# Kernel optimization log

Measured on AMD Instinct MI355X. Metric: run time of the kernel, lower is better.

The kernel has to match this reference:

```python
import jax, jax.numpy as jnp
import numpy as np

NEG_INF = -9e15
NEG_SLOPE = 0.2

def setup_inputs() -> dict:
    key = jax.random.key(0)
    k1, k2, k3, k4 = jax.random.split(key, 4)
    N, d_in, d_out = 8192, 256, 256
    x = jax.random.normal(k1, (N, d_in), dtype=jnp.float32)
    adj = jax.random.randint(k2, (N, N), 0, 2).astype(jnp.float32)
    W = jax.random.normal(k3, (d_in, d_out), dtype=jnp.float32) * (1.0 / np.sqrt(d_in))
    a = jax.random.normal(k4, (2 * d_out,), dtype=jnp.float32) * (1.0 / np.sqrt(2 * d_out))
    return {"x": x, "adj": adj, "W": W, "a": a}

def reference(x, adj, W, a):
    d_out = W.shape[1]
    Wh = x @ W                                   # [N, d_out]
    # a([Wh_i || Wh_j]) decomposed: e_ij = <a_src, Wh_i> + <a_dst, Wh_j>
    e_src = Wh @ a[:d_out]                       # [N]
    e_dst = Wh @ a[d_out:]                       # [N]
    e = jax.nn.leaky_relu(e_src[:, None] + e_dst[None, :], NEG_SLOPE)  # [N, N]
    N = Wh.shape[0]
    mask = (adj > 0) | jnp.eye(N, dtype=bool)
    e = jnp.where(mask, e, NEG_INF)
    alpha = jax.nn.softmax(e, axis=1)            # [N, N]
    h = alpha @ Wh                               # [N, d_out]
    return h
```

## Files before the change

kernel.cpp:

```cpp
#include <hip/hip_runtime.h>
#include <stdint.h>

#define N 8192
#define D 256

typedef __attribute__((ext_vector_type(4))) float f32x4;
typedef __attribute__((ext_vector_type(8))) short bf16x8;

__device__ __forceinline__ unsigned short f2bf(float f) {
    unsigned u = __float_as_uint(f);
    u += 0x7fff + ((u >> 16) & 1);
    return (unsigned short)(u >> 16);
}
__device__ __forceinline__ float leaky(float x) {
    return fmaxf(x, 0.f) + 0.2f * fminf(x, 0.f);
}
__device__ __forceinline__ void sync_lds() {
    asm volatile("s_waitcnt lgkmcnt(0)\n\ts_barrier" ::: "memory");
}

__global__ __launch_bounds__(256) void k0_compress(const float* __restrict__ adj,
                                                   unsigned int* __restrict__ mask) {
    const size_t fbase = ((size_t)blockIdx.x * 256 + threadIdx.x) * 4;
    float4 v = *(const float4*)(adj + fbase);
    const int lane = threadIdx.x & 63;
    unsigned nib = (v.x > 0.f ? 1u : 0u) | (v.y > 0.f ? 2u : 0u) |
                   (v.z > 0.f ? 4u : 0u) | (v.w > 0.f ? 8u : 0u);
    unsigned word = nib << ((lane & 7) * 4);
    word |= __shfl_xor(word, 1);
    word |= __shfl_xor(word, 2);
    word |= __shfl_xor(word, 4);
    if ((lane & 7) == 0) {
        size_t widx = fbase >> 5;
        int r = (int)(widx >> 8);
        int ww = (int)(widx & 255);
        if ((r >> 5) == ww) word |= 1u << (r & 31);
        mask[widx] = word;
    }
}

#define K1_BM 8
__global__ __launch_bounds__(256) void k1_gemm(const float* __restrict__ x,
                                               const float* __restrict__ W,
                                               float* __restrict__ Wh,
                                               unsigned short* __restrict__ WhT) {
    __shared__ float xsT[32][12];
    const int t = threadIdx.x;
    const int r0 = blockIdx.x * K1_BM;
    float acc[K1_BM];
#pragma unroll
    for (int i = 0; i < K1_BM; ++i) acc[i] = 0.f;

    for (int k0 = 0; k0 < D; k0 += 32) {
        __syncthreads();
        if (t < 64) {
            int r = t >> 3, ks = (t & 7) * 4;
            float4 v = *(const float4*)(x + (size_t)(r0 + r) * D + k0 + ks);
            xsT[ks + 0][r] = v.x; xsT[ks + 1][r] = v.y;
            xsT[ks + 2][r] = v.z; xsT[ks + 3][r] = v.w;
        }
        __syncthreads();
#pragma unroll 8
        for (int kk = 0; kk < 32; ++kk) {
            float wv = W[(size_t)(k0 + kk) * D + t];
#pragma unroll
            for (int rc = 0; rc < K1_BM / 4; ++rc) {
                float4 xv = *(const float4*)&xsT[kk][rc * 4];
                acc[rc * 4 + 0] += xv.x * wv;
                acc[rc * 4 + 1] += xv.y * wv;
                acc[rc * 4 + 2] += xv.z * wv;
                acc[rc * 4 + 3] += xv.w * wv;
            }
        }
    }
#pragma unroll
    for (int r = 0; r < K1_BM; ++r) Wh[(size_t)(r0 + r) * D + t] = acc[r];
    unsigned short pk[K1_BM];
#pragma unroll
    for (int r = 0; r < K1_BM; ++r) pk[r] = f2bf(acc[r]);
    uint4* dst = (uint4*)(WhT + (size_t)t * N + r0);
    dst[0] = *(uint4*)&pk[0];
}

__global__ __launch_bounds__(256) void k2_edot(const float* __restrict__ Wh,
                                               const float* __restrict__ a,
                                               float* __restrict__ e_src,
                                               float* __restrict__ e_dst) {
    const int wave = threadIdx.x >> 6, lane = threadIdx.x & 63;
    const int row = blockIdx.x * 4 + wave;
    float4 wv = *(const float4*)(Wh + (size_t)row * D + lane * 4);
    float4 as = *(const float4*)(a + lane * 4);
    float4 ad = *(const float4*)(a + D + lane * 4);
    float ps = wv.x * as.x + wv.y * as.y + wv.z * as.z + wv.w * as.w;
    float pd = wv.x * ad.x + wv.y * ad.y + wv.z * ad.z + wv.w * ad.w;
#pragma unroll
    for (int m = 1; m < 64; m <<= 1) {
        ps += __shfl_xor(ps, m);
        pd += __shfl_xor(pd, m);
    }
    if (lane == 0) { e_src[row] = ps; e_dst[row] = pd; }
}

__global__ __launch_bounds__(256) void k3_max(const float* __restrict__ e_dst,
                                              float* __restrict__ maxdst) {
    __shared__ float red[4];
    const int t = threadIdx.x;
    float m = -3.4e38f;
    for (int i = t; i < N; i += 256) m = fmaxf(m, e_dst[i]);
#pragma unroll
    for (int msk = 1; msk < 64; msk <<= 1) m = fmaxf(m, __shfl_xor(m, msk));
    if ((t & 63) == 0) red[t >> 6] = m;
    __syncthreads();
    if (t == 0) *maxdst = fmaxf(fmaxf(red[0], red[1]), fmaxf(red[2], red[3]));
}

#define BM 64
#define BK 64
#define RB (N / BM)
#define SPLITS 8
#define NITER ((N / SPLITS) / BK)
#define PSTRIDE 72
__global__ __launch_bounds__(512, 4) void k4_main(const unsigned char* __restrict__ mask,
                                                  const unsigned short* __restrict__ WhT,
                                                  const float* __restrict__ e_src,
                                                  const float* __restrict__ e_dst,
                                                  const float* __restrict__ maxdst,
                                                  float* __restrict__ O_part,
                                                  float* __restrict__ l_part) {
    __shared__ unsigned short p_lds[2][BM][PSTRIDE];

    const int t = threadIdx.x;
    const int rb = blockIdx.x & (RB - 1);
    const int s  = blockIdx.x >> 7;
    const int r0 = rb * BM;
    const int j0 = s * (N / SPLITS);

    const int pr = t >> 3;
    const int pcw = t & 7;
    const int pc = pcw * 8;
    const int gr = r0 + pr;

    const int w = t >> 6;
    const int lane = t & 63;
    const int quad = lane >> 4, lo = lane & 15;

    const float md = *maxdst;
    const float es = e_src[gr];
    const float m = leaky(es + md);

    f32x4 acc[4][2];
#pragma unroll
    for (int mt = 0; mt < 4; ++mt)
#pragma unroll
        for (int nt = 0; nt < 2; ++nt)
            acc[mt][nt] = (f32x4){0.f, 0.f, 0.f, 0.f};
    float lsum = 0.f;

    const unsigned char* mrow = mask + (size_t)gr * (N / 8) + (j0 >> 3) + pcw;
    const float* ed_row = e_dst + j0 + pc;
    const unsigned short* wt_base = WhT + (size_t)(w * 32 + lo) * N + j0 + quad * 8;

    unsigned int mb;
    float4 edv0, edv1;
    bf16x8 bfr[2][2];

    mb = mrow[0];
    edv0 = *(const float4*)(ed_row);
    edv1 = *(const float4*)(ed_row + 4);
#pragma unroll
    for (int ks2 = 0; ks2 < 2; ++ks2)
#pragma unroll
        for (int nt = 0; nt < 2; ++nt)
            bfr[ks2][nt] = *(const bf16x8*)(wt_base + (size_t)nt * (16 * N) + ks2 * 32);

    auto stage = [&](int buf) {
        float ev[8] = {edv0.x, edv0.y, edv0.z, edv0.w,
                       edv1.x, edv1.y, edv1.z, edv1.w};
        unsigned short pk[8];
#pragma unroll
        for (int jj = 0; jj < 8; ++jj) {
            float e = leaky(es + ev[jj]);
            float p = ((mb >> jj) & 1u) ? __expf(e - m) : 0.f;
            lsum += p;
            pk[jj] = f2bf(p);
        }
        *(uint4*)&p_lds[buf][pr][pc] = *(uint4*)pk;
    };

    stage(0);
    mb = mrow[8];
    edv0 = *(const float4*)(ed_row + BK);
    edv1 = *(const float4*)(ed_row + BK + 4);
    sync_lds();

#pragma unroll 2
    for (int it = 0; it < NITER; ++it) {
        const int cb = it & 1, nb = cb ^ 1;

#pragma unroll
        for (int ks2 = 0; ks2 < 2; ++ks2) {
            bf16x8 afr[4];
#pragma unroll
            for (int mt = 0; mt < 4; ++mt)
                afr[mt] = *(const bf16x8*)&p_lds[cb][mt * 16 + lo][ks2 * 32 + quad * 8];
#pragma unroll
            for (int nt = 0; nt < 2; ++nt)
#pragma unroll
                for (int mt = 0; mt < 4; ++mt)
                    acc[mt][nt] = __builtin_amdgcn_mfma_f32_16x16x32_bf16(
                        afr[mt], bfr[ks2][nt], acc[mt][nt], 0, 0, 0);
        }

        {
            const int itn = (it + 1 < NITER) ? it + 1 : NITER - 1;
#pragma unroll
            for (int ks2 = 0; ks2 < 2; ++ks2)
#pragma unroll
                for (int nt = 0; nt < 2; ++nt)
                    bfr[ks2][nt] = *(const bf16x8*)(wt_base + (size_t)nt * (16 * N) +
                                                    itn * BK + ks2 * 32);
        }

        if (it + 1 < NITER) {
            stage(nb);
            const int itn2 = (it + 2 < NITER) ? it + 2 : NITER - 1;
            mb = mrow[itn2 * 8];
            edv0 = *(const float4*)(ed_row + itn2 * BK);
            edv1 = *(const float4*)(ed_row + itn2 * BK + 4);
        }
        sync_lds();
    }

#pragma unroll
    for (int msk = 1; msk < 8; msk <<= 1) lsum += __shfl_xor(lsum, msk);
    if ((t & 7) == 0) l_part[(size_t)s * N + gr] = lsum;

    float* obuf = (float*)p_lds;
#pragma unroll
    for (int mt = 0; mt < 4; ++mt) {
        __syncthreads();
#pragma unroll
        for (int nt = 0; nt < 2; ++nt) {
            f32x4 v = acc[mt][nt];
            int col = w * 32 + nt * 16 + lo;
#pragma unroll
            for (int reg = 0; reg < 4; ++reg)
                obuf[(quad * 4 + reg) * 256 + col] = v[reg];
        }
        __syncthreads();
        const int orow = t >> 5;
        const int ocol = (t & 31) * 8;
        f32x4 o0 = *(const f32x4*)&obuf[orow * 256 + ocol];
        f32x4 o1 = *(const f32x4*)&obuf[orow * 256 + ocol + 4];
        float* dst = O_part + ((size_t)s * N + r0 + mt * 16 + orow) * D + ocol;
        *(f32x4*)dst = o0;
        *(f32x4*)(dst + 4) = o1;
    }
}

__global__ __launch_bounds__(256) void k5_reduce(const float* __restrict__ O_part,
                                                 const float* __restrict__ l_part,
                                                 float* __restrict__ out) {
    const int idx = blockIdx.x * 256 + threadIdx.x;
    const int r = idx >> 6;
    float lsum = 0.f;
#pragma unroll
    for (int s = 0; s < SPLITS; ++s) lsum += l_part[(size_t)s * N + r];
    f32x4 o = (f32x4){0.f, 0.f, 0.f, 0.f};
#pragma unroll
    for (int s = 0; s < SPLITS; ++s)
        o += *(const f32x4*)(O_part + (size_t)s * N * D + (size_t)idx * 4);
    const float inv = 1.f / lsum;
    *(f32x4*)(out + (size_t)idx * 4) = o * inv;
}

extern "C" void kernel_launch(void* const* d_in, const int* in_sizes, int n_in,
                              void* d_out, int out_size, void* d_ws, size_t ws_size,
                              hipStream_t stream) {
    const float* x   = (const float*)d_in[0];
    const float* adj = (const float*)d_in[1];
    const float* W   = (const float*)d_in[2];
    const float* a   = (const float*)d_in[3];
    float* out = (float*)d_out;

    char* ws = (char*)d_ws;
    float* Wh            = (float*)(ws);
    unsigned short* WhT  = (unsigned short*)(ws + 8388608);
    float* e_src         = (float*)(ws + 12582912);
    float* e_dst         = (float*)(ws + 12615680);
    float* maxdst        = (float*)(ws + 12648448);
    float* l_part        = (float*)(ws + 12648704);
    unsigned int* mask   = (unsigned int*)(ws + 13631488);
    float* O_part        = (float*)(ws + 25165824);

    k0_compress<<<N * N / 4 / 256, 256, 0, stream>>>(adj, mask);
    k1_gemm<<<N / K1_BM, 256, 0, stream>>>(x, W, Wh, WhT);
    k2_edot<<<N / 4, 256, 0, stream>>>(Wh, a, e_src, e_dst);
    k3_max<<<1, 256, 0, stream>>>(e_dst, maxdst);
    k4_main<<<RB * SPLITS, 512, 0, stream>>>((const unsigned char*)mask, WhT, e_src, e_dst,
                                             maxdst, O_part, l_part);
    k5_reduce<<<N * D / 4 / 256, 256, 0, stream>>>(O_part, l_part, out);
}
```

Before: 484.7 us.

## Double the main kernel K-tile to 128 and drop LDS staging in projection GEMM

The attention kernel now processes 128 neighbour columns per iteration instead of 64. Each thread stages 16 probabilities, and twice as many MFMAs run between barriers, which halves the number of barriers and loop iterations. The projection GEMM loads x rows directly into registers instead of transposing them through shared memory, which removes its syncthreads. The changes raise register and LDS use per block and may lower occupancy under launch_bounds(512,4).

```diff
diff --git a/kernel.cpp b/kernel.cpp
--- a/kernel.cpp
+++ b/kernel.cpp
@@ -44,33 +44,25 @@
                                                const float* __restrict__ W,
                                                float* __restrict__ Wh,
                                                unsigned short* __restrict__ WhT) {
-    __shared__ float xsT[32][12];
     const int t = threadIdx.x;
     const int r0 = blockIdx.x * K1_BM;
     float acc[K1_BM];
 #pragma unroll
     for (int i = 0; i < K1_BM; ++i) acc[i] = 0.f;
 
-    for (int k0 = 0; k0 < D; k0 += 32) {
-        __syncthreads();
-        if (t < 64) {
-            int r = t >> 3, ks = (t & 7) * 4;
-            float4 v = *(const float4*)(x + (size_t)(r0 + r) * D + k0 + ks);
-            xsT[ks + 0][r] = v.x; xsT[ks + 1][r] = v.y;
-            xsT[ks + 2][r] = v.z; xsT[ks + 3][r] = v.w;
-        }
-        __syncthreads();
-#pragma unroll 8
-        for (int kk = 0; kk < 32; ++kk) {
+    for (int k0 = 0; k0 < D; k0 += 8) {
+        float xs[K1_BM][8];
+#pragma unroll
+        for (int r = 0; r < K1_BM; ++r)
+#pragma unroll
+            for (int kk = 0; kk < 8; ++kk)
+                xs[r][kk] = x[(size_t)(r0 + r) * D + k0 + kk];
+#pragma unroll
+        for (int kk = 0; kk < 8; ++kk) {
             float wv = W[(size_t)(k0 + kk) * D + t];
 #pragma unroll
-            for (int rc = 0; rc < K1_BM / 4; ++rc) {
-                float4 xv = *(const float4*)&xsT[kk][rc * 4];
-                acc[rc * 4 + 0] += xv.x * wv;
-                acc[rc * 4 + 1] += xv.y * wv;
-                acc[rc * 4 + 2] += xv.z * wv;
-                acc[rc * 4 + 3] += xv.w * wv;
-            }
+            for (int r = 0; r < K1_BM; ++r)
+                acc[r] += xs[r][kk] * wv;
         }
     }
 #pragma unroll
@@ -78,8 +70,7 @@
     unsigned short pk[K1_BM];
 #pragma unroll
     for (int r = 0; r < K1_BM; ++r) pk[r] = f2bf(acc[r]);
-    uint4* dst = (uint4*)(WhT + (size_t)t * N + r0);
-    dst[0] = *(uint4*)&pk[0];
+    *(uint4*)(WhT + (size_t)t * N + r0) = *(uint4*)&pk[0];
 }
 
 __global__ __launch_bounds__(256) void k2_edot(const float* __restrict__ Wh,
@@ -115,11 +106,11 @@
 }
 
 #define BM 64
-#define BK 64
+#define BK 128
 #define RB (N / BM)
 #define SPLITS 8
 #define NITER ((N / SPLITS) / BK)
-#define PSTRIDE 72
+#define PSTRIDE 136
 __global__ __launch_bounds__(512, 4) void k4_main(const unsigned char* __restrict__ mask,
                                                   const unsigned short* __restrict__ WhT,
                                                   const float* __restrict__ e_src,
@@ -137,7 +128,7 @@
 
     const int pr = t >> 3;
     const int pcw = t & 7;
-    const int pc = pcw * 8;
+    const int pc = pcw * 16;
     const int gr = r0 + pr;
 
     const int w = t >> 6;
@@ -156,41 +147,46 @@
             acc[mt][nt] = (f32x4){0.f, 0.f, 0.f, 0.f};
     float lsum = 0.f;
 
-    const unsigned char* mrow = mask + (size_t)gr * (N / 8) + (j0 >> 3) + pcw;
+    const unsigned char* mrow = mask + (size_t)gr * (N / 8) + (j0 >> 3) + pcw * 2;
     const float* ed_row = e_dst + j0 + pc;
     const unsigned short* wt_base = WhT + (size_t)(w * 32 + lo) * N + j0 + quad * 8;
 
     unsigned int mb;
-    float4 edv0, edv1;
-    bf16x8 bfr[2][2];
-
-    mb = mrow[0];
-    edv0 = *(const float4*)(ed_row);
-    edv1 = *(const float4*)(ed_row + 4);
-#pragma unroll
-    for (int ks2 = 0; ks2 < 2; ++ks2)
+    float4 edv[4];
+    bf16x8 bfr[4][2];
+
+    mb = *(const unsigned short*)(mrow);
+#pragma unroll
+    for (int j = 0; j < 4; ++j) edv[j] = *(const float4*)(ed_row + j * 4);
+#pragma unroll
+    for (int ks = 0; ks < 4; ++ks)
 #pragma unroll
         for (int nt = 0; nt < 2; ++nt)
-            bfr[ks2][nt] = *(const bf16x8*)(wt_base + (size_t)nt * (16 * N) + ks2 * 32);
+            bfr[ks][nt] = *(const bf16x8*)(wt_base + (size_t)nt * (16 * N) + ks * 32);
 
     auto stage = [&](int buf) {
-        float ev[8] = {edv0.x, edv0.y, edv0.z, edv0.w,
-                       edv1.x, edv1.y, edv1.z, edv1.w};
-        unsigned short pk[8];
-#pragma unroll
-        for (int jj = 0; jj < 8; ++jj) {
+        float ev[16];
+#pragma unroll
+        for (int j = 0; j < 4; ++j) {
+            ev[j * 4 + 0] = edv[j].x; ev[j * 4 + 1] = edv[j].y;
+            ev[j * 4 + 2] = edv[j].z; ev[j * 4 + 3] = edv[j].w;
+        }
+        unsigned short pk[16];
+#pragma unroll
+        for (int jj = 0; jj < 16; ++jj) {
             float e = leaky(es + ev[jj]);
             float p = ((mb >> jj) & 1u) ? __expf(e - m) : 0.f;
             lsum += p;
             pk[jj] = f2bf(p);
         }
-        *(uint4*)&p_lds[buf][pr][pc] = *(uint4*)pk;
+        *(uint4*)&p_lds[buf][pr][pc] = *(uint4*)&pk[0];
+        *(uint4*)&p_lds[buf][pr][pc + 8] = *(uint4*)&pk[8];
     };
 
     stage(0);
-    mb = mrow[8];
-    edv0 = *(const float4*)(ed_row + BK);
-    edv1 = *(const float4*)(ed_row + BK + 4);
+    mb = *(const unsigned short*)(mrow + 16);
+#pragma unroll
+    for (int j = 0; j < 4; ++j) edv[j] = *(const float4*)(ed_row + BK + j * 4);
     sync_lds();
 
 #pragma unroll 2
@@ -198,35 +194,36 @@
         const int cb = it & 1, nb = cb ^ 1;
 
 #pragma unroll
-        for (int ks2 = 0; ks2 < 2; ++ks2) {
+        for (int ks = 0; ks < 4; ++ks) {
             bf16x8 afr[4];
 #pragma unroll
             for (int mt = 0; mt < 4; ++mt)
-                afr[mt] = *(const bf16x8*)&p_lds[cb][mt * 16 + lo][ks2 * 32 + quad * 8];
+                afr[mt] = *(const bf16x8*)&p_lds[cb][mt * 16 + lo][ks * 32 + quad * 8];
 #pragma unroll
             for (int nt = 0; nt < 2; ++nt)
 #pragma unroll
                 for (int mt = 0; mt < 4; ++mt)
                     acc[mt][nt] = __builtin_amdgcn_mfma_f32_16x16x32_bf16(
-                        afr[mt], bfr[ks2][nt], acc[mt][nt], 0, 0, 0);
+                        afr[mt], bfr[ks][nt], acc[mt][nt], 0, 0, 0);
         }
 
         {
             const int itn = (it + 1 < NITER) ? it + 1 : NITER - 1;
 #pragma unroll
-            for (int ks2 = 0; ks2 < 2; ++ks2)
+            for (int ks = 0; ks < 4; ++ks)
 #pragma unroll
                 for (int nt = 0; nt < 2; ++nt)
-                    bfr[ks2][nt] = *(const bf16x8*)(wt_base + (size_t)nt * (16 * N) +
-                                                    itn * BK + ks2 * 32);
+                    bfr[ks][nt] = *(const bf16x8*)(wt_base + (size_t)nt * (16 * N) +
+                                                   itn * BK + ks * 32);
         }
 
         if (it + 1 < NITER) {
             stage(nb);
             const int itn2 = (it + 2 < NITER) ? it + 2 : NITER - 1;
-            mb = mrow[itn2 * 8];
-            edv0 = *(const float4*)(ed_row + itn2 * BK);
-            edv1 = *(const float4*)(ed_row + itn2 * BK + 4);
+            mb = *(const unsigned short*)(mrow + itn2 * 16);
+#pragma unroll
+            for (int j = 0; j < 4; ++j)
+                edv[j] = *(const float4*)(ed_row + itn2 * BK + j * 4);
         }
         sync_lds();
     }
```

Result: slower. 517.2 us (+6.7%).

## Compute x@W with split-bf16 MFMA and fuse attention-score dot products

Applied to the files above, without the earlier changes.

Replaces the scalar FP32 x@W GEMM with a bf16 MFMA GEMM. Each operand is split into hi and lo bf16 parts and three MFMAs are used to keep near-FP32 accuracy. The e_src/e_dst dot products are fused into the GEMM epilogue through LDS, so the separate edot kernel and the FP32 Wh round trip go away. This adds two small conversion kernels and extra workspace traffic for the split operands. The GEMM is a small share of total time, since the main attention kernel dominates.

```diff
diff --git a/kernel.cpp b/kernel.cpp
--- a/kernel.cpp
+++ b/kernel.cpp
@@ -11,6 +11,10 @@
     unsigned u = __float_as_uint(f);
     u += 0x7fff + ((u >> 16) & 1);
     return (unsigned short)(u >> 16);
+}
+__device__ __forceinline__ float bf2f(unsigned short h) {
+    unsigned u = ((unsigned)h) << 16;
+    return __uint_as_float(u);
 }
 __device__ __forceinline__ float leaky(float x) {
     return fmaxf(x, 0.f) + 0.2f * fminf(x, 0.f);
@@ -39,66 +43,112 @@
     }
 }
 
-#define K1_BM 8
-__global__ __launch_bounds__(256) void k1_gemm(const float* __restrict__ x,
-                                               const float* __restrict__ W,
-                                               float* __restrict__ Wh,
-                                               unsigned short* __restrict__ WhT) {
-    __shared__ float xsT[32][12];
+__global__ __launch_bounds__(256) void k1c_x(const float* __restrict__ x,
+                                             unsigned short* __restrict__ xhi,
+                                             unsigned short* __restrict__ xlo) {
+    const size_t idx = ((size_t)blockIdx.x * 256 + threadIdx.x) * 4;
+    float4 v = *(const float4*)(x + idx);
+    unsigned short h[4], l[4];
+    float vv[4] = {v.x, v.y, v.z, v.w};
+#pragma unroll
+    for (int j = 0; j < 4; ++j) {
+        h[j] = f2bf(vv[j]);
+        l[j] = f2bf(vv[j] - bf2f(h[j]));
+    }
+    *(ushort4*)(xhi + idx) = *(ushort4*)h;
+    *(ushort4*)(xlo + idx) = *(ushort4*)l;
+}
+
+__global__ __launch_bounds__(256) void k1w(const float* __restrict__ W,
+                                           unsigned short* __restrict__ wthi,
+                                           unsigned short* __restrict__ wtlo) {
+    const int n = blockIdx.x;
+    const int k = threadIdx.x;
+    float w = W[(size_t)k * D + n];
+    unsigned short h = f2bf(w);
+    unsigned short l = f2bf(w - bf2f(h));
+    wthi[(size_t)n * D + k] = h;
+    wtlo[(size_t)n * D + k] = l;
+}
+
+__global__ __launch_bounds__(256) void k1m(const unsigned short* __restrict__ xhi,
+                                           const unsigned short* __restrict__ xlo,
+                                           const unsigned short* __restrict__ wthi,
+                                           const unsigned short* __restrict__ wtlo,
+                                           const float* __restrict__ a,
+                                           unsigned short* __restrict__ WhT,
+                                           float* __restrict__ e_src,
+                                           float* __restrict__ e_dst) {
+    __shared__ float obuf[16 * 256];
+
     const int t = threadIdx.x;
-    const int r0 = blockIdx.x * K1_BM;
-    float acc[K1_BM];
-#pragma unroll
-    for (int i = 0; i < K1_BM; ++i) acc[i] = 0.f;
-
-    for (int k0 = 0; k0 < D; k0 += 32) {
-        __syncthreads();
-        if (t < 64) {
-            int r = t >> 3, ks = (t & 7) * 4;
-            float4 v = *(const float4*)(x + (size_t)(r0 + r) * D + k0 + ks);
-            xsT[ks + 0][r] = v.x; xsT[ks + 1][r] = v.y;
-            xsT[ks + 2][r] = v.z; xsT[ks + 3][r] = v.w;
-        }
-        __syncthreads();
-#pragma unroll 8
-        for (int kk = 0; kk < 32; ++kk) {
-            float wv = W[(size_t)(k0 + kk) * D + t];
-#pragma unroll
-            for (int rc = 0; rc < K1_BM / 4; ++rc) {
-                float4 xv = *(const float4*)&xsT[kk][rc * 4];
-                acc[rc * 4 + 0] += xv.x * wv;
-                acc[rc * 4 + 1] += xv.y * wv;
-                acc[rc * 4 + 2] += xv.z * wv;
-                acc[rc * 4 + 3] += xv.w * wv;
-            }
-        }
-    }
-#pragma unroll
-    for (int r = 0; r < K1_BM; ++r) Wh[(size_t)(r0 + r) * D + t] = acc[r];
-    unsigned short pk[K1_BM];
-#pragma unroll
-    for (int r = 0; r < K1_BM; ++r) pk[r] = f2bf(acc[r]);
-    uint4* dst = (uint4*)(WhT + (size_t)t * N + r0);
-    dst[0] = *(uint4*)&pk[0];
-}
-
-__global__ __launch_bounds__(256) void k2_edot(const float* __restrict__ Wh,
-                                               const float* __restrict__ a,
-                                               float* __restrict__ e_src,
-                                               float* __restrict__ e_dst) {
-    const int wave = threadIdx.x >> 6, lane = threadIdx.x & 63;
-    const int row = blockIdx.x * 4 + wave;
-    float4 wv = *(const float4*)(Wh + (size_t)row * D + lane * 4);
-    float4 as = *(const float4*)(a + lane * 4);
-    float4 ad = *(const float4*)(a + D + lane * 4);
-    float ps = wv.x * as.x + wv.y * as.y + wv.z * as.z + wv.w * as.w;
-    float pd = wv.x * ad.x + wv.y * ad.y + wv.z * ad.z + wv.w * ad.w;
-#pragma unroll
-    for (int m = 1; m < 64; m <<= 1) {
-        ps += __shfl_xor(ps, m);
-        pd += __shfl_xor(pd, m);
-    }
-    if (lane == 0) { e_src[row] = ps; e_dst[row] = pd; }
+    const int r0 = blockIdx.x * 16;
+    const int w = t >> 6;
+    const int lane = t & 63;
+    const int quad = lane >> 4, lo = lane & 15;
+
+    const unsigned short* xh_row = xhi + (size_t)(r0 + lo) * D;
+    const unsigned short* xl_row = xlo + (size_t)(r0 + lo) * D;
+
+    f32x4 acc[4];
+#pragma unroll
+    for (int nt = 0; nt < 4; ++nt) acc[nt] = (f32x4){0.f, 0.f, 0.f, 0.f};
+
+#pragma unroll
+    for (int ks = 0; ks < 8; ++ks) {
+        const int kofs = ks * 32 + quad * 8;
+        bf16x8 ah = *(const bf16x8*)(xh_row + kofs);
+        bf16x8 al = *(const bf16x8*)(xl_row + kofs);
+#pragma unroll
+        for (int nt = 0; nt < 4; ++nt) {
+            const int n = w * 64 + nt * 16 + lo;
+            bf16x8 bh = *(const bf16x8*)(wthi + (size_t)n * D + kofs);
+            bf16x8 bl = *(const bf16x8*)(wtlo + (size_t)n * D + kofs);
+            acc[nt] = __builtin_amdgcn_mfma_f32_16x16x32_bf16(ah, bh, acc[nt], 0, 0, 0);
+            acc[nt] = __builtin_amdgcn_mfma_f32_16x16x32_bf16(ah, bl, acc[nt], 0, 0, 0);
+            acc[nt] = __builtin_amdgcn_mfma_f32_16x16x32_bf16(al, bh, acc[nt], 0, 0, 0);
+        }
+    }
+
+#pragma unroll
+    for (int nt = 0; nt < 4; ++nt) {
+        const int n = w * 64 + nt * 16 + lo;
+        unsigned short pk[4];
+#pragma unroll
+        for (int reg = 0; reg < 4; ++reg) pk[reg] = f2bf(acc[nt][reg]);
+        *(ushort2*)(WhT + (size_t)n * N + r0 + quad * 4) = *(ushort2*)&pk[0];
+        *(ushort2*)(WhT + (size_t)n * N + r0 + quad * 4 + 2) = *(ushort2*)&pk[2];
+    }
+
+#pragma unroll
+    for (int nt = 0; nt < 4; ++nt) {
+        const int col = w * 64 + nt * 16 + lo;
+#pragma unroll
+        for (int reg = 0; reg < 4; ++reg)
+            obuf[(quad * 4 + reg) * 256 + col] = acc[nt][reg];
+    }
+    __syncthreads();
+
+    const int row = t >> 4;
+    const int c0 = (t & 15) * 16;
+    float ps = 0.f, pd = 0.f;
+#pragma unroll
+    for (int j = 0; j < 4; ++j) {
+        float4 wv = *(const float4*)&obuf[row * 256 + c0 + j * 4];
+        float4 as = *(const float4*)(a + c0 + j * 4);
+        float4 ad = *(const float4*)(a + D + c0 + j * 4);
+        ps += wv.x * as.x + wv.y * as.y + wv.z * as.z + wv.w * as.w;
+        pd += wv.x * ad.x + wv.y * ad.y + wv.z * ad.z + wv.w * ad.w;
+    }
+#pragma unroll
+    for (int msk = 1; msk < 16; msk <<= 1) {
+        ps += __shfl_xor(ps, msk);
+        pd += __shfl_xor(pd, msk);
+    }
+    if ((t & 15) == 0) {
+        e_src[r0 + row] = ps;
+        e_dst[r0 + row] = pd;
+    }
 }
 
 __global__ __launch_bounds__(256) void k3_max(const float* __restrict__ e_dst,
@@ -284,18 +334,22 @@
     float* out = (float*)d_out;
 
     char* ws = (char*)d_ws;
-    float* Wh            = (float*)(ws);
+    unsigned short* xhi  = (unsigned short*)(ws);
+    unsigned short* xlo  = (unsigned short*)(ws + 4194304);
     unsigned short* WhT  = (unsigned short*)(ws + 8388608);
-    float* e_src         = (float*)(ws + 12582912);
-    float* e_dst         = (float*)(ws + 12615680);
-    float* maxdst        = (float*)(ws + 12648448);
-    float* l_part        = (float*)(ws + 12648704);
+    unsigned short* wthi = (unsigned short*)(ws + 12582912);
+    unsigned short* wtlo = (unsigned short*)(ws + 12713984);
+    float* e_src         = (float*)(ws + 12845056);
+    float* e_dst         = (float*)(ws + 12877824);
+    float* maxdst        = (float*)(ws + 12910592);
+    float* l_part        = (float*)(ws + 12910848);
     unsigned int* mask   = (unsigned int*)(ws + 13631488);
     float* O_part        = (float*)(ws + 25165824);
 
     k0_compress<<<N * N / 4 / 256, 256, 0, stream>>>(adj, mask);
-    k1_gemm<<<N / K1_BM, 256, 0, stream>>>(x, W, Wh, WhT);
-    k2_edot<<<N / 4, 256, 0, stream>>>(Wh, a, e_src, e_dst);
+    k1c_x<<<N * D / 4 / 256, 256, 0, stream>>>(x, xhi, xlo);
+    k1w<<<D, D, 0, stream>>>(W, wthi, wtlo);
+    k1m<<<N / 16, 256, 0, stream>>>(xhi, xlo, wthi, wtlo, a, WhT, e_src, e_dst);
     k3_max<<<1, 256, 0, stream>>>(e_dst, maxdst);
     k4_main<<<RB * SPLITS, 512, 0, stream>>>((const unsigned char*)mask, WhT, e_src, e_dst,
                                              maxdst, O_part, l_part);
```

After: 482.8 us. No clear change (-0.4%).
